# Performance work log

Measured on AMD Instinct MI355X. Metric: run time of the kernel, lower is better.

## Reference

```python
import math
import jax, jax.numpy as jnp
import numpy as np

B = 128          # batch_size (graphs)
SEQ = 128        # max_seq_len (nodes per graph)
D = 128          # input_dim
HID = 64         # enc_hidden_dim
HEADS = 4        # in_head
N = B * SEQ      # total nodes
E = 262144       # edges (avg degree 16)


def _make_pe(seq, d):
    pos = np.arange(seq, dtype=np.float32)[:, None]
    i_even = np.arange(0, d, 2, dtype=np.float32)
    pe = np.zeros((seq, d), dtype=np.float32)
    pe[:, 0::2] = np.sin(pos / 10000.0 ** (2.0 * i_even / d))
    pe[:, 1::2] = np.cos(pos / 10000.0 ** (2.0 * (i_even + 1.0) / d))
    return jnp.asarray(pe)


def setup_inputs() -> dict:
    key = jax.random.key(0)
    ks = jax.random.split(key, 10)
    s = 0.1
    return {
        "x": jax.random.normal(ks[0], (N, D), jnp.float32),
        "edge_index": jax.random.randint(ks[1], (2, E), 0, N),
        "pe": _make_pe(SEQ, D),
        "W1": jax.random.normal(ks[2], (D, HEADS * HID), jnp.float32) * s,
        "a_src1": jax.random.normal(ks[3], (HEADS, HID), jnp.float32) * s,
        "a_dst1": jax.random.normal(ks[4], (HEADS, HID), jnp.float32) * s,
        "b1": jnp.zeros((HEADS * HID,), jnp.float32),
        "W2": jax.random.normal(ks[5], (HEADS * HID, HID), jnp.float32) * s,
        "a_src2": jax.random.normal(ks[6], (1, HID), jnp.float32) * s,
        "a_dst2": jax.random.normal(ks[7], (1, HID), jnp.float32) * s,
        "b2": jnp.zeros((HID,), jnp.float32),
        "batch_size": B,
    }


def _gat_conv(x, src, dst, W, a_src, a_dst, b, heads, ch, concat, n):
    # PyG GATConv (eval mode, self-loops already appended to src/dst).
    h = (x @ W).reshape(n, heads, ch)                      # [N,H,C]
    alpha_src = jnp.einsum("nhc,hc->nh", h, a_src)         # [N,H]
    alpha_dst = jnp.einsum("nhc,hc->nh", h, a_dst)
    e = jax.nn.leaky_relu(alpha_src[src] + alpha_dst[dst], 0.2)  # [E,H]
    m = jax.ops.segment_max(e, dst, num_segments=n)        # segment softmax over dst
    ex = jnp.exp(e - m[dst])
    den = jax.ops.segment_sum(ex, dst, num_segments=n)
    alpha = ex / (den[dst] + 1e-16)                        # [E,H]
    out = jax.ops.segment_sum(h[src] * alpha[:, :, None], dst, num_segments=n)
    out = out.reshape(n, heads * ch) if concat else out.mean(axis=1)
    return out + b


def reference(x, edge_index, pe, W1, a_src1, a_dst1, b1, W2, a_src2, a_dst2, b2, batch_size):
    n = x.shape[0]
    loop = jnp.arange(n)
    src = jnp.concatenate([edge_index[0], loop])           # add self-loops (PyG default)
    dst = jnp.concatenate([edge_index[1], loop])
    # positional encoding (dropout inactive in eval)
    h = x * math.sqrt(x.shape[1]) + jnp.tile(pe, (batch_size, 1))
    h = jax.nn.elu(_gat_conv(h, src, dst, W1, a_src1, a_dst1, b1, HEADS, HID, True, n))
    out = _gat_conv(h, src, dst, W2, a_src2, a_dst2, b2, 1, HID, False, n)
    return out.reshape(batch_size, -1, out.shape[1])
```

## Files before the change

kernel.cpp:

```cpp
#include <hip/hip_runtime.h>
#include <hip/hip_bf16.h>

typedef __hip_bfloat16 bf16;

#define N_NODES 16384
#define D_IN    128
#define HID     64
#define HEADS   4
#define F1      256
#define SEQ     128
#define SLOTS   64

__device__ __forceinline__ float wave_sum(float v) {
    #pragma unroll
    for (int o = 32; o > 0; o >>= 1) v += __shfl_xor(v, o, 64);
    return v;
}
__device__ __forceinline__ float lrelu(float v) { return v > 0.f ? v : 0.2f * v; }
__device__ __forceinline__ float rdlane(float v, int l) {
    return __uint_as_float(__builtin_amdgcn_readlane(__float_as_uint(v), l));
}

#define UNPACK8(u, te, acc)                                          \
    do {                                                             \
        acc[0] += (te) * __uint_as_float((u).x << 16);               \
        acc[1] += (te) * __uint_as_float((u).x & 0xffff0000u);       \
        acc[2] += (te) * __uint_as_float((u).y << 16);               \
        acc[3] += (te) * __uint_as_float((u).y & 0xffff0000u);       \
        acc[4] += (te) * __uint_as_float((u).z << 16);               \
        acc[5] += (te) * __uint_as_float((u).z & 0xffff0000u);       \
        acc[6] += (te) * __uint_as_float((u).w << 16);               \
        acc[7] += (te) * __uint_as_float((u).w & 0xffff0000u);       \
    } while (0)

__global__ __launch_bounds__(256) void k_gemm1z(const float* __restrict__ x,
                                                const float* __restrict__ pe,
                                                const float* __restrict__ W1,
                                                const float* __restrict__ a_src1,
                                                const float* __restrict__ a_dst1,
                                                bf16* __restrict__ h,
                                                float* __restrict__ as1,
                                                float* __restrict__ ad1,
                                                int4* __restrict__ cntv) {
    int tid = threadIdx.x, lane = tid & 63, wv = tid >> 6;
    if (tid < 4) cntv[blockIdx.x * 4 + tid] = make_int4(0, 0, 0, 0);

    int base = blockIdx.x * 16;
    int j4 = lane * 4;
    float2 xr[4];
    #pragma unroll
    for (int i = 0; i < 4; i++) {
        int row = base + wv * 4 + i;
        float2 xa  = *(const float2*)(x  + (size_t)row * 128 + 2 * lane);
        float2 pea = *(const float2*)(pe + (size_t)(row & (SEQ - 1)) * 128 + 2 * lane);
        xr[i].x = xa.x * 11.313708499f + pea.x;
        xr[i].y = xa.y * 11.313708499f + pea.y;
    }
    float acc[4][4] = {};
    const float4* Wv = (const float4*)W1;
    #pragma unroll 4
    for (int k2 = 0; k2 < 64; k2++) {
        float4 w0 = Wv[(size_t)(2 * k2) * 64 + lane];
        float4 w1 = Wv[(size_t)(2 * k2 + 1) * 64 + lane];
        #pragma unroll
        for (int i = 0; i < 4; i++) {
            float a0 = rdlane(xr[i].x, k2);
            float a1 = rdlane(xr[i].y, k2);
            acc[i][0] += a0 * w0.x + a1 * w1.x;
            acc[i][1] += a0 * w0.y + a1 * w1.y;
            acc[i][2] += a0 * w0.z + a1 * w1.z;
            acc[i][3] += a0 * w0.w + a1 * w1.w;
        }
    }
    float4 asv = *(const float4*)(a_src1 + j4);
    float4 adv = *(const float4*)(a_dst1 + j4);
    #pragma unroll
    for (int i = 0; i < 4; i++) {
        int row = base + wv * 4 + i;
        union { bf16 b[4]; ushort4 u; } cv;
        cv.b[0] = __float2bfloat16(acc[i][0]);
        cv.b[1] = __float2bfloat16(acc[i][1]);
        cv.b[2] = __float2bfloat16(acc[i][2]);
        cv.b[3] = __float2bfloat16(acc[i][3]);
        *(ushort4*)(h + (size_t)row * 256 + j4) = cv.u;
        float vs = acc[i][0] * asv.x + acc[i][1] * asv.y + acc[i][2] * asv.z + acc[i][3] * asv.w;
        float vd = acc[i][0] * adv.x + acc[i][1] * adv.y + acc[i][2] * adv.z + acc[i][3] * adv.w;
        #pragma unroll
        for (int o = 1; o < 16; o <<= 1) {
            vs += __shfl_xor(vs, o);
            vd += __shfl_xor(vd, o);
        }
        if ((lane & 15) == 0) {
            as1[row * 4 + (lane >> 4)] = vs;
            ad1[row * 4 + (lane >> 4)] = vd;
        }
    }
}

__global__ __launch_bounds__(256) void k_scatter(const int* __restrict__ ei, int E, int Etot,
                                                 int* __restrict__ cnt,
                                                 int* __restrict__ esrc) {
    int e = blockIdx.x * 256 + threadIdx.x;
    if (e >= Etot) return;
    int s, d;
    if (e < E) { s = ei[e]; d = ei[E + e]; }
    else       { s = e - E; d = s; }
    int pos = atomicAdd(&cnt[d], 1);
    if (pos < SLOTS) esrc[d * SLOTS + pos] = s;
}

__global__ __launch_bounds__(256) void k_agg1_gemm2(
        const int* __restrict__ cnt, const int* __restrict__ esrc,
        const bf16* __restrict__ h,
        const float* __restrict__ as1, const float* __restrict__ ad1,
        const float* __restrict__ b1,
        const float* __restrict__ W2,
        const float* __restrict__ a_src2, const float* __restrict__ a_dst2,
        bf16* __restrict__ h2, float* __restrict__ as2, float* __restrict__ ad2) {
    __shared__ float hs[8][256];
    __shared__ float part[4][8][64];
    int tid = threadIdx.x, lane = tid & 63, wv = tid >> 6;
    int dbase = blockIdx.x * 8;

    int eg = lane >> 3;
    int cg_ = lane & 7;
    const bf16* hbase = h + (size_t)wv * 64 + cg_ * 8;

    #pragma unroll 2
    for (int it = 0; it < 8; it++) {
        int d = dbase + it;
        int deg = min(cnt[d], SLOTS);
        float adw = ad1[d * 4 + wv];

        int s = 0; float t = 0.f;
        if (lane < deg) {
            s = esrc[d * SLOTS + lane];
            t = __expf(lrelu(as1[s * 4 + wv] + adw) - 40.f);
        }

        float acc[8] = {0, 0, 0, 0, 0, 0, 0, 0};
        for (int sub = 0; sub < deg; sub += 32) {
            int qn = (min(deg - sub, 32) + 7) >> 3;
            int se0, se1, se2, se3; float te0, te1, te2, te3;
            uint4 u0, u1, u2, u3;
            se0 = __shfl(s, sub + eg);      te0 = __shfl(t, sub + eg);
            u0 = *(const uint4*)(hbase + (size_t)se0 * 256);
            if (qn > 1) {
                se1 = __shfl(s, sub + 8 + eg);  te1 = __shfl(t, sub + 8 + eg);
                u1 = *(const uint4*)(hbase + (size_t)se1 * 256);
            }
            if (qn > 2) {
                se2 = __shfl(s, sub + 16 + eg); te2 = __shfl(t, sub + 16 + eg);
                u2 = *(const uint4*)(hbase + (size_t)se2 * 256);
            }
            if (qn > 3) {
                se3 = __shfl(s, sub + 24 + eg); te3 = __shfl(t, sub + 24 + eg);
                u3 = *(const uint4*)(hbase + (size_t)se3 * 256);
            }
            UNPACK8(u0, te0, acc);
            if (qn > 1) UNPACK8(u1, te1, acc);
            if (qn > 2) UNPACK8(u2, te2, acc);
            if (qn > 3) UNPACK8(u3, te3, acc);
        }
        #pragma unroll
        for (int j = 0; j < 8; j++) {
            acc[j] += __shfl_xor(acc[j], 8);
            acc[j] += __shfl_xor(acc[j], 16);
            acc[j] += __shfl_xor(acc[j], 32);
        }
        float den = wave_sum(t);
        if (lane < 8) {
            float inv = 1.f / den;
            int cbase = wv * 64 + lane * 8;
            float o[8];
            #pragma unroll
            for (int j = 0; j < 8; j++) {
                float v = acc[j] * inv + b1[cbase + j];
                o[j] = v > 0.f ? v : (__expf(v) - 1.f);
            }
            float4* dst = (float4*)&hs[it][cbase];
            dst[0] = make_float4(o[0], o[1], o[2], o[3]);
            dst[1] = make_float4(o[4], o[5], o[6], o[7]);
        }
    }
    __syncthreads();

    {
        float acc2[8] = {0, 0, 0, 0, 0, 0, 0, 0};
        const int k4base = wv * 16;
        for (int kk = 0; kk < 16; kk++) {
            int k4 = k4base + kk;
            const float* wp = W2 + (size_t)k4 * 256 + lane;
            float w0 = wp[0], w1 = wp[64], w2 = wp[128], w3 = wp[192];
            #pragma unroll
            for (int r = 0; r < 8; r++) {
                float4 u = *(const float4*)&hs[r][k4 * 4];
                acc2[r] += u.x * w0 + u.y * w1 + u.z * w2 + u.w * w3;
            }
        }
        #pragma unroll
        for (int r = 0; r < 8; r++) part[wv][r][lane] = acc2[r];
    }
    __syncthreads();
    {
        int r0 = wv * 2, r1 = r0 + 1;
        float a0 = part[0][r0][lane] + part[1][r0][lane] + part[2][r0][lane] + part[3][r0][lane];
        float a1 = part[0][r1][lane] + part[1][r1][lane] + part[2][r1][lane] + part[3][r1][lane];
        float asj = a_src2[lane], adj = a_dst2[lane];
        int n0 = dbase + r0, n1 = dbase + r1;
        h2[(size_t)n0 * 64 + lane] = __float2bfloat16(a0);
        h2[(size_t)n1 * 64 + lane] = __float2bfloat16(a1);
        float va0 = wave_sum(a0 * asj);
        float vd0 = wave_sum(a0 * adj);
        float va1 = wave_sum(a1 * asj);
        float vd1 = wave_sum(a1 * adj);
        if (lane == 0) {
            as2[n0] = va0; ad2[n0] = vd0;
            as2[n1] = va1; ad2[n1] = vd1;
        }
    }
}

__global__ __launch_bounds__(256) void k_agg2(const int* __restrict__ cnt,
                                              const int* __restrict__ esrc,
                                              const bf16* __restrict__ h2,
                                              const float* __restrict__ as2,
                                              const float* __restrict__ ad2,
                                              const float* __restrict__ b2v,
                                              float* __restrict__ out) {
    int tid = threadIdx.x, lane = tid & 63, wv = tid >> 6;
    int d = blockIdx.x * 4 + wv;
    int deg = min(cnt[d], SLOTS);
    float adw = ad2[d];
    int eg = lane >> 3, cg_ = lane & 7;
    const bf16* hbase = h2 + cg_ * 8;

    int s = 0; float t = 0.f;
    if (lane < deg) {
        s = esrc[d * SLOTS + lane];
        t = __expf(lrelu(as2[s] + adw) - 40.f);
    }

    float acc[8] = {0, 0, 0, 0, 0, 0, 0, 0};
    for (int sub = 0; sub < deg; sub += 32) {
        int qn = (min(deg - sub, 32) + 7) >> 3;
        int se0, se1, se2, se3; float te0, te1, te2, te3;
        uint4 u0, u1, u2, u3;
        se0 = __shfl(s, sub + eg);      te0 = __shfl(t, sub + eg);
        u0 = *(const uint4*)(hbase + (size_t)se0 * 64);
        if (qn > 1) {
            se1 = __shfl(s, sub + 8 + eg);  te1 = __shfl(t, sub + 8 + eg);
            u1 = *(const uint4*)(hbase + (size_t)se1 * 64);
        }
        if (qn > 2) {
            se2 = __shfl(s, sub + 16 + eg); te2 = __shfl(t, sub + 16 + eg);
            u2 = *(const uint4*)(hbase + (size_t)se2 * 64);
        }
        if (qn > 3) {
            se3 = __shfl(s, sub + 24 + eg); te3 = __shfl(t, sub + 24 + eg);
            u3 = *(const uint4*)(hbase + (size_t)se3 * 64);
        }
        UNPACK8(u0, te0, acc);
        if (qn > 1) UNPACK8(u1, te1, acc);
        if (qn > 2) UNPACK8(u2, te2, acc);
        if (qn > 3) UNPACK8(u3, te3, acc);
    }
    #pragma unroll
    for (int j = 0; j < 8; j++) {
        acc[j] += __shfl_xor(acc[j], 8);
        acc[j] += __shfl_xor(acc[j], 16);
        acc[j] += __shfl_xor(acc[j], 32);
    }
    float den = wave_sum(t);
    if (lane < 8) {
        float inv = 1.f / den;
        int cbase = lane * 8;
        float o[8];
        #pragma unroll
        for (int j = 0; j < 8; j++) o[j] = acc[j] * inv + b2v[cbase + j];
        float4* dst = (float4*)(out + (size_t)d * 64 + cbase);
        dst[0] = make_float4(o[0], o[1], o[2], o[3]);
        dst[1] = make_float4(o[4], o[5], o[6], o[7]);
    }
}

extern "C" void kernel_launch(void* const* d_in, const int* in_sizes, int n_in,
                              void* d_out, int out_size, void* d_ws, size_t ws_size,
                              hipStream_t stream) {
    const float* x    = (const float*)d_in[0];
    const int*   ei   = (const int*)  d_in[1];
    const float* pe   = (const float*)d_in[2];
    const float* W1   = (const float*)d_in[3];
    const float* a_s1 = (const float*)d_in[4];
    const float* a_d1 = (const float*)d_in[5];
    const float* b1   = (const float*)d_in[6];
    const float* W2   = (const float*)d_in[7];
    const float* a_s2 = (const float*)d_in[8];
    const float* a_d2 = (const float*)d_in[9];
    const float* b2   = (const float*)d_in[10];

    const int E    = in_sizes[1] / 2;
    const int n    = N_NODES;
    const int Etot = E + n;

    char* p = (char*)d_ws;
    auto alloc = [&](size_t bytes) -> void* {
        void* r = (void*)p;
        p += (bytes + 255) & ~(size_t)255;
        return r;
    };
    int*   cnt     = (int*)  alloc((size_t)n * 4);
    int*   esrc    = (int*)  alloc((size_t)n * SLOTS * 4);
    bf16*  h       = (bf16*) alloc((size_t)n * F1 * 2);
    float* as1     = (float*)alloc((size_t)n * HEADS * 4);
    float* ad1     = (float*)alloc((size_t)n * HEADS * 4);
    bf16*  h2      = (bf16*) alloc((size_t)n * HID * 2);
    float* as2     = (float*)alloc((size_t)n * 4);
    float* ad2     = (float*)alloc((size_t)n * 4);

    int eblocks = (Etot + 255) / 256;

    k_gemm1z    <<<n / 16, 256, 0, stream>>>(x, pe, W1, a_s1, a_d1, h, as1, ad1, (int4*)cnt);
    k_scatter   <<<eblocks, 256, 0, stream>>>(ei, E, Etot, cnt, esrc);
    k_agg1_gemm2<<<n / 8, 256, 0, stream>>>(cnt, esrc, h, as1, ad1, b1,
                                            W2, a_s2, a_d2, h2, as2, ad2);
    k_agg2      <<<n / 4, 256, 0, stream>>>(cnt, esrc, h2, as2, ad2, b2, (float*)d_out);
}
```

Before: 173.5 us.

## Precompute layer-1 edge attention weights during scatter into slot-major buffer

The scatter kernel now gathers the per-head source and destination attention logits and writes the exp(leaky_relu) edge weights into a per-destination, per-head slot array. The layer-1 aggregation then reads these contiguously instead of doing a dependent gather of as1 per edge. The aggregation kernels also load esrc unconditionally with a mask, rather than behind a degree branch, and load the block's degrees once with a shuffle. The cost is an extra 16 MB scratch buffer and more scattered writes in the scatter kernel. Stale slots are read but zeroed by the degree check.

```diff
diff --git a/kernel.cpp b/kernel.cpp
--- a/kernel.cpp
+++ b/kernel.cpp
@@ -99,20 +99,32 @@
 
 __global__ __launch_bounds__(256) void k_scatter(const int* __restrict__ ei, int E, int Etot,
                                                  int* __restrict__ cnt,
-                                                 int* __restrict__ esrc) {
+                                                 int* __restrict__ esrc,
+                                                 const float* __restrict__ as1,
+                                                 const float* __restrict__ ad1,
+                                                 float* __restrict__ et) {
     int e = blockIdx.x * 256 + threadIdx.x;
     if (e >= Etot) return;
     int s, d;
     if (e < E) { s = ei[e]; d = ei[E + e]; }
     else       { s = e - E; d = s; }
     int pos = atomicAdd(&cnt[d], 1);
-    if (pos < SLOTS) esrc[d * SLOTS + pos] = s;
+    if (pos < SLOTS) {
+        esrc[d * SLOTS + pos] = s;
+        float4 av = *(const float4*)(as1 + (size_t)s * 4);
+        float4 bv = *(const float4*)(ad1 + (size_t)d * 4);
+        size_t eb = (size_t)d * 4 * SLOTS + pos;
+        et[eb + 0 * SLOTS] = __expf(lrelu(av.x + bv.x) - 40.f);
+        et[eb + 1 * SLOTS] = __expf(lrelu(av.y + bv.y) - 40.f);
+        et[eb + 2 * SLOTS] = __expf(lrelu(av.z + bv.z) - 40.f);
+        et[eb + 3 * SLOTS] = __expf(lrelu(av.w + bv.w) - 40.f);
+    }
 }
 
 __global__ __launch_bounds__(256) void k_agg1_gemm2(
         const int* __restrict__ cnt, const int* __restrict__ esrc,
+        const float* __restrict__ et,
         const bf16* __restrict__ h,
-        const float* __restrict__ as1, const float* __restrict__ ad1,
         const float* __restrict__ b1,
         const float* __restrict__ W2,
         const float* __restrict__ a_src2, const float* __restrict__ a_dst2,
@@ -126,17 +138,15 @@
     int cg_ = lane & 7;
     const bf16* hbase = h + (size_t)wv * 64 + cg_ * 8;
 
+    int cv = cnt[dbase + (lane & 7)];
+
     #pragma unroll 2
     for (int it = 0; it < 8; it++) {
         int d = dbase + it;
-        int deg = min(cnt[d], SLOTS);
-        float adw = ad1[d * 4 + wv];
-
-        int s = 0; float t = 0.f;
-        if (lane < deg) {
-            s = esrc[d * SLOTS + lane];
-            t = __expf(lrelu(as1[s * 4 + wv] + adw) - 40.f);
-        }
+        int deg = min(__shfl(cv, it), SLOTS);
+        int s = esrc[(size_t)d * SLOTS + lane] & (N_NODES - 1);
+        float tv = et[((size_t)d * 4 + wv) * SLOTS + lane];
+        float t = (lane < deg) ? tv : 0.f;
 
         float acc[8] = {0, 0, 0, 0, 0, 0, 0, 0};
         for (int sub = 0; sub < deg; sub += 32) {
@@ -235,11 +245,9 @@
     int eg = lane >> 3, cg_ = lane & 7;
     const bf16* hbase = h2 + cg_ * 8;
 
-    int s = 0; float t = 0.f;
-    if (lane < deg) {
-        s = esrc[d * SLOTS + lane];
-        t = __expf(lrelu(as2[s] + adw) - 40.f);
-    }
+    int s = esrc[(size_t)d * SLOTS + lane] & (N_NODES - 1);
+    float ev = as2[s];
+    float t = (lane < deg) ? __expf(lrelu(ev + adw) - 40.f) : 0.f;
 
     float acc[8] = {0, 0, 0, 0, 0, 0, 0, 0};
     for (int sub = 0; sub < deg; sub += 32) {
@@ -311,6 +319,7 @@
     };
     int*   cnt     = (int*)  alloc((size_t)n * 4);
     int*   esrc    = (int*)  alloc((size_t)n * SLOTS * 4);
+    float* et      = (float*)alloc((size_t)n * HEADS * SLOTS * 4);
     bf16*  h       = (bf16*) alloc((size_t)n * F1 * 2);
     float* as1     = (float*)alloc((size_t)n * HEADS * 4);
     float* ad1     = (float*)alloc((size_t)n * HEADS * 4);
@@ -321,8 +330,8 @@
     int eblocks = (Etot + 255) / 256;
 
     k_gemm1z    <<<n / 16, 256, 0, stream>>>(x, pe, W1, a_s1, a_d1, h, as1, ad1, (int4*)cnt);
-    k_scatter   <<<eblocks, 256, 0, stream>>>(ei, E, Etot, cnt, esrc);
-    k_agg1_gemm2<<<n / 8, 256, 0, stream>>>(cnt, esrc, h, as1, ad1, b1,
+    k_scatter   <<<eblocks, 256, 0, stream>>>(ei, E, Etot, cnt, esrc, as1, ad1, et);
+    k_agg1_gemm2<<<n / 8, 256, 0, stream>>>(cnt, esrc, et, h, b1,
                                             W2, a_s2, a_d2, h2, as2, ad2);
     k_agg2      <<<n / 4, 256, 0, stream>>>(cnt, esrc, h2, as2, ad2, b2, (float*)d_out);
 }
```

New measurement: 183.5 us. +5.7%, slower.
